# Kernel optimization log

Hardware: AMD Instinct MI355X
Metric: run time of the kernel (lower is better)

## Reference

```python
import jax, jax.numpy as jnp
import numpy as np

# tanh-approximate GELU, matching F.gelu(..., approximate='tanh')
_SQRT_2_OVER_PI = 0.7978845608028654

def gelu_tanh(x):
    return 0.5 * x * (1.0 + jnp.tanh(_SQRT_2_OVER_PI * (x + 0.044715 * x * x * x)))

def setup_inputs() -> dict:
    key = jax.random.key(0)
    k1, k2, k3 = jax.random.split(key, 3)
    E, T, H, F = 8, 2048, 1024, 4096
    x = jax.random.normal(k1, (E, T, H), dtype=jnp.float32)
    w1 = jax.random.normal(k2, (E, H, F), dtype=jnp.float32) * (1.0 / np.sqrt(H))
    w2 = jax.random.normal(k3, (E, F, H), dtype=jnp.float32) * (1.0 / np.sqrt(F))
    return {"x": x, "w1": w1, "w2": w2}

def reference(x, w1, w2):
    # [E,T,H] @ [E,H,F] -> [E,T,F]
    h = jnp.einsum('eth,ehf->etf', x, w1)
    h = gelu_tanh(h)
    # [E,T,F] @ [E,F,H] -> [E,T,H]
    return jnp.einsum('etf,efh->eth', h, w2)
```

## Files before the change

kernel.cpp:

```cpp
#include <hip/hip_runtime.h>
#include <hip/hip_bf16.h>

typedef __attribute__((ext_vector_type(8))) short short8;
typedef __attribute__((ext_vector_type(8))) unsigned short ushort8;
typedef __attribute__((ext_vector_type(4))) float f32x4;

typedef const __attribute__((address_space(1))) void* as1cv_t;
typedef __attribute__((address_space(3))) void* as3v_t;
typedef __attribute__((address_space(3))) const char* as3cc_t;
typedef __attribute__((address_space(3))) const short8* as3s8_t;

__device__ __forceinline__ unsigned short f2bf(float f) {
    unsigned u = __float_as_uint(f);
    u += 0x7fffu + ((u >> 16) & 1u);
    return (unsigned short)(u >> 16);
}

__device__ __forceinline__ float gelu_tanh_f(float x) {
    float t = 0.7978845608028654f * (x + 0.044715f * x * x * x);
    float u = 2.0f * t;
    u = fminf(fmaxf(u, -30.0f), 30.0f);
    float e = __expf(u);
    float th = (e - 1.0f) / (e + 1.0f);
    return 0.5f * x * (1.0f + th);
}

__device__ __forceinline__ void tr64body(const float* ine, unsigned short* oute,
                                         int R, int C, int c0, int r0, int t,
                                         float* LT) {
#pragma unroll
    for (int q = 0; q < 4; ++q) {
        int f = q * 256 + t;
        int lr = f >> 4;
        int lc4 = f & 15;
        float4 v = *(const float4*)(ine + (size_t)(r0 + lr) * C + c0 + lc4 * 4);
        LT[(lc4 * 4 + 0) * 65 + lr] = v.x;
        LT[(lc4 * 4 + 1) * 65 + lr] = v.y;
        LT[(lc4 * 4 + 2) * 65 + lr] = v.z;
        LT[(lc4 * 4 + 3) * 65 + lr] = v.w;
    }
    __syncthreads();
#pragma unroll
    for (int s = 0; s < 2; ++s) {
        int oc = t >> 2;
        int or8 = (t & 3) + s * 4;
        const float* src = &LT[oc * 65 + or8 * 8];
        ushort8 o;
#pragma unroll
        for (int j = 0; j < 8; ++j) o[j] = f2bf(src[j]);
        *(ushort8*)(oute + (size_t)(c0 + oc) * R + r0 + or8 * 8) = o;
    }
}

__global__ void prep_all(const float* __restrict__ x,
                         const float* __restrict__ w1,
                         const float* __restrict__ w2,
                         unsigned short* __restrict__ xb,
                         unsigned short* __restrict__ w1t,
                         unsigned short* __restrict__ w2t) {
    __shared__ float LT[64 * 65];
    const int E = 8, T = 2048, H = 1024, F = 4096;
    int bid = blockIdx.x;
    int t = threadIdx.x;
    if (bid < 8192) {
        int cx = bid & 63, rest = bid >> 6;
        int ry = rest & 15, e = rest >> 4;
        tr64body(w1 + (size_t)e * H * F, w1t + (size_t)e * H * F,
                 H, F, cx * 64, ry * 64, t, LT);
    } else if (bid < 16384) {
        int b = bid - 8192;
        int cx = b & 15, rest = b >> 4;
        int ry = rest & 63, e = rest >> 6;
        tr64body(w2 + (size_t)e * F * H, w2t + (size_t)e * F * H,
                 F, H, cx * 64, ry * 64, t, LT);
    } else {
        int b = bid - 16384;
        long long i = (long long)b * 256 + t;
        long long stride = 2048LL * 256;
        const float4* in4 = (const float4*)x;
        ushort4* out4 = (ushort4*)xb;
        long long n4 = ((long long)E * T * H) >> 2;
        for (long long j = i; j < n4; j += stride) {
            float4 v = in4[j];
            ushort4 o;
            o.x = f2bf(v.x); o.y = f2bf(v.y); o.z = f2bf(v.z); o.w = f2bf(v.w);
            out4[j] = o;
        }
    }
}

__device__ __forceinline__ void gload16(const void* g, void* l) {
    __builtin_amdgcn_global_load_lds((as1cv_t)g, (as3v_t)l, 16, 0, 0);
}

#define MFMA_BF16 __builtin_amdgcn_mfma_f32_16x16x32_bf16
#define FENCE() asm volatile("" ::: "memory")

template <int DO_GELU, int ROUNDS>
__device__ __forceinline__ void gemm_body(
    const unsigned short* __restrict__ A,
    const unsigned short* __restrict__ Bt,
    void* __restrict__ Cout,
    int M, int N, int K, int bmw_count, int per_e, int nwg)
{
    int bid = blockIdx.x;
    int gbid = (bid & 7) * (nwg >> 3) + (bid >> 3);
    int e  = gbid / per_e;
    int t0_ = gbid % per_e;
    int bn  = t0_ / bmw_count;
    int sub = t0_ % bmw_count;
    int bm0 = sub * ROUNDS;

    const size_t K2 = (size_t)K * 2;
    const char* Ae = (const char*)A  + ((size_t)e * M * K + (size_t)bm0 * 256 * K) * 2;
    const char* Be = (const char*)Bt + ((size_t)e * N * K + (size_t)bn  * 256 * K) * 2;

    __shared__ alignas(16) unsigned short lds[2 * 32768];
    char* ldsc = (char*)lds;
    as3cc_t lb = (as3cc_t)(const char*)lds;

    int tid  = threadIdx.x;
    int wid  = tid >> 6;
    int lane = tid & 63;
    int wave_m = wid >> 2;
    int wave_n = wid & 3;

    int srow = wid * 8 + (lane >> 3);
    int kbsw = ((lane & 7) ^ (srow & 7)) << 4;
    const char* gA = Ae + (size_t)srow * K2 + kbsw;
    const char* gB = Be + (size_t)srow * K2 + kbsw;
    const size_t HROW = 64 * K2;
    const size_t HALF = 128 * K2;
    int sOff = wid << 10;

    unsigned kg   = (unsigned)(lane >> 4);
    unsigned keyl = (unsigned)((lane & 15) & 7);
    unsigned sl0  = (kg ^ keyl) << 4;
    unsigned aoff = (unsigned)(wave_m * 16384 + (lane & 15) * 128) + sl0;
    unsigned boff = 32768u + (unsigned)((wave_n >> 1) * 16384 +
                    ((wave_n & 1) * 64 + (lane & 15)) * 128) + sl0;

    f32x4 acc[8][4];
    f32x4 zero = {0.0f, 0.0f, 0.0f, 0.0f};
#pragma unroll
    for (int i = 0; i < 8; i++)
#pragma unroll
        for (int j = 0; j < 4; j++) acc[i][j] = zero;

    const int KT = K >> 6;
    const int NT_TOT = ROUNDS * KT;
    const size_t AROUND = 255 * K2;

    int kA = 0, kB = 0;
#define ADV_A() do { gA += 128; if (++kA == KT) { kA = 0; gA += AROUND; } } while (0)
#define ADV_B() do { gB += 128; if (++kB == KT) { kB = 0; gB -= K2; } } while (0)

#define STG_A(h, r, bufbit) gload16(gA + (h) * HALF + (r) * HROW, \
        ldsc + ((bufbit) << 16) + (h) * 16384 + (r) * 8192 + sOff)
#define STG_B(h, r, bufbit) gload16(gB + (h) * HALF + (r) * HROW, \
        ldsc + ((bufbit) << 16) + 32768 + (h) * 16384 + (r) * 8192 + sOff)

    STG_A(0, 0, 0); STG_A(0, 1, 0); STG_A(1, 0, 0); STG_A(1, 1, 0);
    STG_B(0, 0, 0); STG_B(0, 1, 0); STG_B(1, 0, 0); STG_B(1, 1, 0);
    ADV_B();
    if (NT_TOT > 1) {
        STG_B(0, 0, 1); STG_B(0, 1, 1); STG_B(1, 0, 1); STG_B(1, 1, 1);
        asm volatile("s_waitcnt vmcnt(4)" ::: "memory");
    } else {
        asm volatile("s_waitcnt vmcnt(0)" ::: "memory");
    }
    ADV_B();
    ADV_A();
    __builtin_amdgcn_s_barrier();
    FENCE();

    int ktEp = 0, rEp = 0;

    for (int t = 0; t < NT_TOT; ++t) {
        unsigned bufR = (unsigned)(t & 1) << 16;
        int wbA = (t + 1) & 1;
        int wbB = t & 1;
        bool stA = (t + 1) < NT_TOT;
        bool stB = (t + 2) < NT_TOT;

        unsigned pa0 = bufR + aoff, pa1 = pa0 ^ 64u;
        unsigned pb0 = bufR + boff, pb1 = pb0 ^ 64u;

        short8 aL[4][2], aH[4][2], bL[2][2], bH[2][2];

#pragma unroll
        for (int mi = 0; mi < 4; ++mi) {
            aL[mi][0] = *(as3s8_t)(lb + (pa0 + mi * 2048));
            aL[mi][1] = *(as3s8_t)(lb + (pa1 + mi * 2048));
        }
#pragma unroll
        for (int ni = 0; ni < 2; ++ni) {
            bL[ni][0] = *(as3s8_t)(lb + (pb0 + ni * 2048));
            bL[ni][1] = *(as3s8_t)(lb + (pb1 + ni * 2048));
        }
        if (stA) { STG_A(0, 0, wbA); STG_A(0, 1, wbA); }
        FENCE();
        __builtin_amdgcn_s_barrier();
        FENCE();
        __builtin_amdgcn_s_setprio(1);
#pragma unroll
        for (int ks = 0; ks < 2; ++ks)
#pragma unroll
            for (int mi = 0; mi < 4; ++mi)
#pragma unroll
                for (int ni = 0; ni < 2; ++ni)
                    acc[mi][ni] = MFMA_BF16(aL[mi][ks], bL[ni][ks], acc[mi][ni], 0, 0, 0);
        __builtin_amdgcn_s_setprio(0);
        FENCE();
        __builtin_amdgcn_s_barrier();
        FENCE();

#pragma unroll
        for (int ni = 0; ni < 2; ++ni) {
            bH[ni][0] = *(as3s8_t)(lb + (pb0 + (2 + ni) * 2048));
            bH[ni][1] = *(as3s8_t)(lb + (pb1 + (2 + ni) * 2048));
        }
        if (stA) { STG_A(1, 0, wbA); STG_A(1, 1, wbA); }
        ADV_A();
        FENCE();
        __builtin_amdgcn_s_barrier();
        FENCE();
        __builtin_amdgcn_s_setprio(1);
#pragma unroll
        for (int ks = 0; ks < 2; ++ks)
#pragma unroll
            for (int mi = 0; mi < 4; ++mi)
#pragma unroll
                for (int ni = 0; ni < 2; ++ni)
                    acc[mi][2 + ni] = MFMA_BF16(aL[mi][ks], bH[ni][ks], acc[mi][2 + ni], 0, 0, 0);
        __builtin_amdgcn_s_setprio(0);
        FENCE();
        __builtin_amdgcn_s_barrier();
        FENCE();

#pragma unroll
        for (int mi = 0; mi < 4; ++mi) {
            aH[mi][0] = *(as3s8_t)(lb + (pa0 + (4 + mi) * 2048));
            aH[mi][1] = *(as3s8_t)(lb + (pa1 + (4 + mi) * 2048));
        }
        if (stB) { STG_B(0, 0, wbB); STG_B(0, 1, wbB); }
        FENCE();
        __builtin_amdgcn_s_barrier();
        FENCE();
        __builtin_amdgcn_s_setprio(1);
#pragma unroll
        for (int ks = 0; ks < 2; ++ks)
#pragma unroll
            for (int mi = 0; mi < 4; ++mi)
#pragma unroll
                for (int ni = 0; ni < 2; ++ni)
                    acc[4 + mi][2 + ni] = MFMA_BF16(aH[mi][ks], bH[ni][ks], acc[4 + mi][2 + ni], 0, 0, 0);
        __builtin_amdgcn_s_setprio(0);
        FENCE();
        __builtin_amdgcn_s_barrier();
        FENCE();

        if (stB) { STG_B(1, 0, wbB); STG_B(1, 1, wbB); }
        ADV_B();
        if (stB) asm volatile("s_waitcnt vmcnt(4)" ::: "memory");
        else     asm volatile("s_waitcnt vmcnt(0)" ::: "memory");
        __builtin_amdgcn_s_barrier();
        FENCE();
        __builtin_amdgcn_s_setprio(1);
#pragma unroll
        for (int ks = 0; ks < 2; ++ks)
#pragma unroll
            for (int mi = 0; mi < 4; ++mi)
#pragma unroll
                for (int ni = 0; ni < 2; ++ni)
                    acc[4 + mi][ni] = MFMA_BF16(aH[mi][ks], bL[ni][ks], acc[4 + mi][ni], 0, 0, 0);
        __builtin_amdgcn_s_setprio(0);
        FENCE();
        __builtin_amdgcn_s_barrier();
        FENCE();

        if (++ktEp == KT) {
            ktEp = 0;
            int row0 = (bm0 + rEp) * 256 + wave_m * 128 + ((lane >> 4) << 2);
            int col0 = bn * 256 + wave_n * 64 + (lane & 15);
            if (DO_GELU) {
                unsigned short* Ce = (unsigned short*)Cout + (size_t)e * M * N;
#pragma unroll
                for (int m = 0; m < 8; ++m)
#pragma unroll
                    for (int n = 0; n < 4; ++n)
#pragma unroll
                        for (int j = 0; j < 4; ++j) {
                            int row = row0 + m * 16 + j;
                            int col = col0 + n * 16;
                            Ce[(size_t)row * N + col] = f2bf(gelu_tanh_f(acc[m][n][j]));
                        }
            } else {
                float* Ce = (float*)Cout + (size_t)e * M * N;
#pragma unroll
                for (int m = 0; m < 8; ++m)
#pragma unroll
                    for (int n = 0; n < 4; ++n)
#pragma unroll
                        for (int j = 0; j < 4; ++j) {
                            int row = row0 + m * 16 + j;
                            int col = col0 + n * 16;
                            Ce[(size_t)row * N + col] = acc[m][n][j];
                        }
            }
            rEp++;
#pragma unroll
            for (int i = 0; i < 8; i++)
#pragma unroll
                for (int j = 0; j < 4; j++) acc[i][j] = zero;
        }
    }
#undef STG_A
#undef STG_B
#undef ADV_A
#undef ADV_B
}

__global__ __launch_bounds__(512, 2) void gemm_mlp1(
    const unsigned short* __restrict__ A, const unsigned short* __restrict__ Bt,
    void* __restrict__ C, int M, int N, int K, int bmw, int per_e, int nwg) {
    gemm_body<1, 4>(A, Bt, C, M, N, K, bmw, per_e, nwg);
}
__global__ __launch_bounds__(512, 2) void gemm_mlp2(
    const unsigned short* __restrict__ A, const unsigned short* __restrict__ Bt,
    void* __restrict__ C, int M, int N, int K, int bmw, int per_e, int nwg) {
    gemm_body<0, 1>(A, Bt, C, M, N, K, bmw, per_e, nwg);
}

extern "C" void kernel_launch(void* const* d_in, const int* in_sizes, int n_in,
                              void* d_out, int out_size, void* d_ws, size_t ws_size,
                              hipStream_t stream) {
    const float* x  = (const float*)d_in[0];
    const float* w1 = (const float*)d_in[1];
    const float* w2 = (const float*)d_in[2];
    float* out = (float*)d_out;

    const int E = 8, T = 2048, H = 1024, F = 4096;

    unsigned short* xb  = (unsigned short*)d_ws;
    unsigned short* w1t = xb  + (size_t)E * T * H;
    unsigned short* w2t = w1t + (size_t)E * H * F;
    unsigned short* hb  = w2t + (size_t)E * F * H;

    prep_all<<<18432, 256, 0, stream>>>(x, w1, w2, xb, w1t, w2t);

    {
        int M_ = T, N_ = F, K_ = H;
        int bmw = (M_ / 256) / 4;
        int per_e = (N_ / 256) * bmw;
        int nwg = E * per_e;
        gemm_mlp1<<<nwg, 512, 0, stream>>>(xb, w1t, hb, M_, N_, K_, bmw, per_e, nwg);
    }
    {
        int M_ = T, N_ = H, K_ = F;
        int bmw = M_ / 256;
        int per_e = (N_ / 256) * bmw;
        int nwg = E * per_e;
        gemm_mlp2<<<nwg, 512, 0, stream>>>(hb, w2t, out, M_, N_, K_, bmw, per_e, nwg);
    }
}
```

Baseline: 380.2 us.

## Switch GEMM inner loop from 16x16x32 to 32x32x16 bf16 MFMA

Replaces the 16x16x32 MFMA tiling with 32x32x16 MFMA tiles. The LDS fragment loads, swizzle offsets, accumulator layout and epilogue store indexing are rewritten to match. Each wave still covers a 128x64 output tile per k-step, now with fewer, larger MFMA instructions and a different LDS read pattern. The aim is to cut instruction issue overhead and LDS traffic per FLOP. The risk is different register pressure, possible LDS bank conflicts with the new swizzle, and correctness of the fragment mapping.

```diff
diff --git a/kernel.cpp b/kernel.cpp
--- a/kernel.cpp
+++ b/kernel.cpp
@@ -3,7 +3,7 @@
 
 typedef __attribute__((ext_vector_type(8))) short short8;
 typedef __attribute__((ext_vector_type(8))) unsigned short ushort8;
-typedef __attribute__((ext_vector_type(4))) float f32x4;
+typedef __attribute__((ext_vector_type(16))) float f32x16;
 
 typedef const __attribute__((address_space(1))) void* as1cv_t;
 typedef __attribute__((address_space(3))) void* as3v_t;
@@ -93,7 +93,7 @@
     __builtin_amdgcn_global_load_lds((as1cv_t)g, (as3v_t)l, 16, 0, 0);
 }
 
-#define MFMA_BF16 __builtin_amdgcn_mfma_f32_16x16x32_bf16
+#define MFMA32 __builtin_amdgcn_mfma_f32_32x32x16_bf16
 #define FENCE() asm volatile("" ::: "memory")
 
 template <int DO_GELU, int ROUNDS>
@@ -133,19 +133,24 @@
     const size_t HALF = 128 * K2;
     int sOff = wid << 10;
 
-    unsigned kg   = (unsigned)(lane >> 4);
-    unsigned keyl = (unsigned)((lane & 15) & 7);
-    unsigned sl0  = (kg ^ keyl) << 4;
-    unsigned aoff = (unsigned)(wave_m * 16384 + (lane & 15) * 128) + sl0;
-    unsigned boff = 32768u + (unsigned)((wave_n >> 1) * 16384 +
-                    ((wave_n & 1) * 64 + (lane & 15)) * 128) + sl0;
-
-    f32x4 acc[8][4];
-    f32x4 zero = {0.0f, 0.0f, 0.0f, 0.0f};
-#pragma unroll
-    for (int i = 0; i < 8; i++)
-#pragma unroll
-        for (int j = 0; j < 4; j++) acc[i][j] = zero;
+    int r31   = lane & 31;
+    int khalf = lane >> 5;
+    unsigned key  = (unsigned)(lane & 7);
+    unsigned rowA = (unsigned)(wave_m * 16384 + r31 * 128);
+    unsigned rowB = 32768u + (unsigned)((wave_n >> 1) * 16384 +
+                    ((wave_n & 1) * 64 + r31) * 128);
+    unsigned sb[4];
+#pragma unroll
+    for (int ks = 0; ks < 4; ++ks)
+        sb[ks] = (unsigned)(((unsigned)(ks * 2 + khalf) ^ key) << 4);
+
+    f32x16 acc[4][2];
+#pragma unroll
+    for (int i = 0; i < 4; i++)
+#pragma unroll
+        for (int j = 0; j < 2; j++)
+#pragma unroll
+            for (int q = 0; q < 16; q++) acc[i][j][q] = 0.0f;
 
     const int KT = K >> 6;
     const int NT_TOT = ROUNDS * KT;
@@ -183,43 +188,37 @@
         bool stA = (t + 1) < NT_TOT;
         bool stB = (t + 2) < NT_TOT;
 
-        unsigned pa0 = bufR + aoff, pa1 = pa0 ^ 64u;
-        unsigned pb0 = bufR + boff, pb1 = pb0 ^ 64u;
-
-        short8 aL[4][2], aH[4][2], bL[2][2], bH[2][2];
-
-#pragma unroll
-        for (int mi = 0; mi < 4; ++mi) {
-            aL[mi][0] = *(as3s8_t)(lb + (pa0 + mi * 2048));
-            aL[mi][1] = *(as3s8_t)(lb + (pa1 + mi * 2048));
-        }
-#pragma unroll
-        for (int ni = 0; ni < 2; ++ni) {
-            bL[ni][0] = *(as3s8_t)(lb + (pb0 + ni * 2048));
-            bL[ni][1] = *(as3s8_t)(lb + (pb1 + ni * 2048));
-        }
+        unsigned pa = bufR + rowA;
+        unsigned pb = bufR + rowB;
+
+        short8 aF[2][4], aH[2][4], b0[4], b1[4];
+
+#pragma unroll
+        for (int mb = 0; mb < 2; ++mb)
+#pragma unroll
+            for (int ks = 0; ks < 4; ++ks)
+                aF[mb][ks] = *(as3s8_t)(lb + (pa + mb * 4096 + sb[ks]));
+#pragma unroll
+        for (int ks = 0; ks < 4; ++ks)
+            b0[ks] = *(as3s8_t)(lb + (pb + sb[ks]));
         if (stA) { STG_A(0, 0, wbA); STG_A(0, 1, wbA); }
         FENCE();
         __builtin_amdgcn_s_barrier();
         FENCE();
         __builtin_amdgcn_s_setprio(1);
 #pragma unroll
-        for (int ks = 0; ks < 2; ++ks)
-#pragma unroll
-            for (int mi = 0; mi < 4; ++mi)
-#pragma unroll
-                for (int ni = 0; ni < 2; ++ni)
-                    acc[mi][ni] = MFMA_BF16(aL[mi][ks], bL[ni][ks], acc[mi][ni], 0, 0, 0);
+        for (int ks = 0; ks < 4; ++ks)
+#pragma unroll
+            for (int mb = 0; mb < 2; ++mb)
+                acc[mb][0] = MFMA32(aF[mb][ks], b0[ks], acc[mb][0], 0, 0, 0);
         __builtin_amdgcn_s_setprio(0);
         FENCE();
         __builtin_amdgcn_s_barrier();
         FENCE();
 
 #pragma unroll
-        for (int ni = 0; ni < 2; ++ni) {
-            bH[ni][0] = *(as3s8_t)(lb + (pb0 + (2 + ni) * 2048));
-            bH[ni][1] = *(as3s8_t)(lb + (pb1 + (2 + ni) * 2048));
-        }
+        for (int ks = 0; ks < 4; ++ks)
+            b1[ks] = *(as3s8_t)(lb + (pb + 4096 + sb[ks]));
         if (stA) { STG_A(1, 0, wbA); STG_A(1, 1, wbA); }
         ADV_A();
         FENCE();
@@ -227,34 +226,30 @@
         FENCE();
         __builtin_amdgcn_s_setprio(1);
 #pragma unroll
-        for (int ks = 0; ks < 2; ++ks)
-#pragma unroll
-            for (int mi = 0; mi < 4; ++mi)
-#pragma unroll
-                for (int ni = 0; ni < 2; ++ni)
-                    acc[mi][2 + ni] = MFMA_BF16(aL[mi][ks], bH[ni][ks], acc[mi][2 + ni], 0, 0, 0);
+        for (int ks = 0; ks < 4; ++ks)
+#pragma unroll
+            for (int mb = 0; mb < 2; ++mb)
+                acc[mb][1] = MFMA32(aF[mb][ks], b1[ks], acc[mb][1], 0, 0, 0);
         __builtin_amdgcn_s_setprio(0);
         FENCE();
         __builtin_amdgcn_s_barrier();
         FENCE();
 
 #pragma unroll
-        for (int mi = 0; mi < 4; ++mi) {
-            aH[mi][0] = *(as3s8_t)(lb + (pa0 + (4 + mi) * 2048));
-            aH[mi][1] = *(as3s8_t)(lb + (pa1 + (4 + mi) * 2048));
-        }
+        for (int mb = 0; mb < 2; ++mb)
+#pragma unroll
+            for (int ks = 0; ks < 4; ++ks)
+                aH[mb][ks] = *(as3s8_t)(lb + (pa + (2 + mb) * 4096 + sb[ks]));
         if (stB) { STG_B(0, 0, wbB); STG_B(0, 1, wbB); }
         FENCE();
         __builtin_amdgcn_s_barrier();
         FENCE();
         __builtin_amdgcn_s_setprio(1);
 #pragma unroll
-        for (int ks = 0; ks < 2; ++ks)
-#pragma unroll
-            for (int mi = 0; mi < 4; ++mi)
-#pragma unroll
-                for (int ni = 0; ni < 2; ++ni)
-                    acc[4 + mi][2 + ni] = MFMA_BF16(aH[mi][ks], bH[ni][ks], acc[4 + mi][2 + ni], 0, 0, 0);
+        for (int ks = 0; ks < 4; ++ks)
+#pragma unroll
+            for (int mb = 0; mb < 2; ++mb)
+                acc[2 + mb][1] = MFMA32(aH[mb][ks], b1[ks], acc[2 + mb][1], 0, 0, 0);
         __builtin_amdgcn_s_setprio(0);
         FENCE();
         __builtin_amdgcn_s_barrier();
@@ -268,12 +263,10 @@
         FENCE();
         __builtin_amdgcn_s_setprio(1);
 #pragma unroll
-        for (int ks = 0; ks < 2; ++ks)
-#pragma unroll
-            for (int mi = 0; mi < 4; ++mi)
-#pragma unroll
-                for (int ni = 0; ni < 2; ++ni)
-                    acc[4 + mi][ni] = MFMA_BF16(aH[mi][ks], bL[ni][ks], acc[4 + mi][ni], 0, 0, 0);
+        for (int ks = 0; ks < 4; ++ks)
+#pragma unroll
+            for (int mb = 0; mb < 2; ++mb)
+                acc[2 + mb][0] = MFMA32(aH[mb][ks], b0[ks], acc[2 + mb][0], 0, 0, 0);
         __builtin_amdgcn_s_setprio(0);
         FENCE();
         __builtin_amdgcn_s_barrier();
@@ -281,38 +274,40 @@
 
         if (++ktEp == KT) {
             ktEp = 0;
-            int row0 = (bm0 + rEp) * 256 + wave_m * 128 + ((lane >> 4) << 2);
-            int col0 = bn * 256 + wave_n * 64 + (lane & 15);
+            int row0 = (bm0 + rEp) * 256 + wave_m * 128 + ((lane >> 5) << 2);
+            int col0 = bn * 256 + wave_n * 64 + (lane & 31);
             if (DO_GELU) {
                 unsigned short* Ce = (unsigned short*)Cout + (size_t)e * M * N;
 #pragma unroll
-                for (int m = 0; m < 8; ++m)
-#pragma unroll
-                    for (int n = 0; n < 4; ++n)
-#pragma unroll
-                        for (int j = 0; j < 4; ++j) {
-                            int row = row0 + m * 16 + j;
-                            int col = col0 + n * 16;
-                            Ce[(size_t)row * N + col] = f2bf(gelu_tanh_f(acc[m][n][j]));
+                for (int mb = 0; mb < 4; ++mb)
+#pragma unroll
+                    for (int nb = 0; nb < 2; ++nb)
+#pragma unroll
+                        for (int rg = 0; rg < 16; ++rg) {
+                            int row = row0 + mb * 32 + (rg & 3) + 8 * (rg >> 2);
+                            int col = col0 + nb * 32;
+                            Ce[(size_t)row * N + col] = f2bf(gelu_tanh_f(acc[mb][nb][rg]));
                         }
             } else {
                 float* Ce = (float*)Cout + (size_t)e * M * N;
 #pragma unroll
-                for (int m = 0; m < 8; ++m)
-#pragma unroll
-                    for (int n = 0; n < 4; ++n)
-#pragma unroll
-                        for (int j = 0; j < 4; ++j) {
-                            int row = row0 + m * 16 + j;
-                            int col = col0 + n * 16;
-                            Ce[(size_t)row * N + col] = acc[m][n][j];
+                for (int mb = 0; mb < 4; ++mb)
+#pragma unroll
+                    for (int nb = 0; nb < 2; ++nb)
+#pragma unroll
+                        for (int rg = 0; rg < 16; ++rg) {
+                            int row = row0 + mb * 32 + (rg & 3) + 8 * (rg >> 2);
+                            int col = col0 + nb * 32;
+                            Ce[(size_t)row * N + col] = acc[mb][nb][rg];
                         }
             }
             rEp++;
 #pragma unroll
-            for (int i = 0; i < 8; i++)
-#pragma unroll
-                for (int j = 0; j < 4; j++) acc[i][j] = zero;
+            for (int i = 0; i < 4; i++)
+#pragma unroll
+                for (int j = 0; j < 2; j++)
+#pragma unroll
+                    for (int q = 0; q < 16; q++) acc[i][j][q] = 0.0f;
         }
     }
 #undef STG_A
```

Result: slower. 418.5 us (+10.1%).
